# Performance work log

Hardware: AMD Instinct MI355X
Metric: run time of the kernel (lower is better)

The kernel has to match this reference:

```python
import jax, jax.numpy as jnp
import numpy as np


def setup_inputs() -> dict:
    B, C, N = 8, 512, 2048
    ks = jax.random.split(jax.random.key(0), 5)
    return {
        "src_embedding": jax.random.normal(ks[0], (B, C, N), jnp.float32),
        "tgt_embedding": jax.random.normal(ks[1], (B, C, N), jnp.float32),
        "src": jax.random.normal(ks[2], (B, 3, N), jnp.float32),
        "tgt": jax.random.normal(ks[3], (B, 3, N), jnp.float32),
        "temperature": jnp.ones((B, 1), jnp.float32),
        "gumbel_u": jax.random.uniform(ks[4], (B * N, N), jnp.float32),
    }


def reference(src_embedding, tgt_embedding, src, tgt, temperature, gumbel_u):
    B, C, N = src_embedding.shape
    # cross-attention scores: [B, N, N]
    scores = jnp.einsum('bcn,bcm->bnm', src_embedding, tgt_embedding) / jnp.sqrt(jnp.float32(C))
    scores = scores.reshape(B * N, N)
    tau = jnp.repeat(temperature.reshape(B, 1, 1), N, axis=1).reshape(-1, 1)  # [B*N, 1]
    # gumbel-softmax (hard=True, straight-through)
    u = jnp.clip(gumbel_u, 1e-6, 1.0 - 1e-6)
    g = -jnp.log(-jnp.log(u))
    y_soft = jax.nn.softmax((scores + g) / tau, axis=-1)
    idx = jnp.argmax(y_soft, axis=-1)
    y_hard = jax.nn.one_hot(idx, N, dtype=y_soft.dtype)
    scores_st = y_hard - jax.lax.stop_gradient(y_soft) + y_soft
    scores_st = scores_st.reshape(B, N, N)
    # soft correspondences: tgt @ scores^T -> [B, 3, N]
    src_corr = jnp.einsum('bcm,bnm->bcn', tgt, scores_st)
    src_mean = src.mean(axis=2, keepdims=True)
    corr_mean = src_corr.mean(axis=2, keepdims=True)
    src_c = src - src_mean
    corr_c = src_corr - corr_mean
    # 3x3 covariance per batch
    H = jnp.einsum('bcn,bdn->bcd', src_c, corr_c)
    uS, s, vh = jnp.linalg.svd(H)
    v = jnp.swapaxes(vh, -1, -2)
    uT = jnp.swapaxes(uS, -1, -2)
    r = v @ uT
    det = jax.lax.stop_gradient(jnp.linalg.det(r))  # torch code uses .item(): constant
    d = jnp.stack([jnp.ones_like(det), jnp.ones_like(det), det], axis=-1)  # [B, 3]
    R = (v * d[:, None, :]) @ uT  # v @ diag([1,1,det]) @ u^T
    t = jnp.einsum('bij,bjk->bik', -R, src_mean) + corr_mean
    return R, t.reshape(B, 3)
```

## Files before the change

kernel.cpp:

```cpp
#include <hip/hip_runtime.h>
#include <hip/hip_fp16.h>
#include <math.h>

#define NB 8
#define NC 512
#define NN 2048

typedef __attribute__((ext_vector_type(8))) _Float16 f16x8;
typedef __attribute__((ext_vector_type(4))) float f32x4;

union U8 { uint32_t u[4]; f16x8 v; };

__device__ __forceinline__ unsigned f2mono(float v) {
    unsigned b = __float_as_uint(v);
    return (b & 0x80000000u) ? ~b : (b | 0x80000000u);
}

__device__ __forceinline__ uint32_t packsplit(float a) {
    __half h = __float2half(a);
    float hf = __half2float(h);
    __half lo = __float2half(a - hf);
    return (uint32_t)__half_as_ushort(h) | ((uint32_t)__half_as_ushort(lo) << 16);
}

extern "C" __global__ __launch_bounds__(256, 2)
void scores_argmax(const float* __restrict__ srcE,
                   const float* __restrict__ tgtE,
                   const float* __restrict__ gum,
                   const float* __restrict__ temp,
                   unsigned long long* __restrict__ best)
{
    __shared__ uint32_t As[128 * 32];
    __shared__ uint32_t Bs[128 * 32];

    const int id = blockIdx.x;
    const int flat = (id & 7) * 256 + (id >> 3);
    const int mt = flat & 15;
    const int nt = (flat >> 4) & 15;
    const int b  = flat >> 8;
    const int n0 = nt * 128, m0 = mt * 128;

    const int tid = threadIdx.x;
    const int wv = tid >> 6;
    const int l  = tid & 63;
    const int wn = wv >> 1, wm = wv & 1;
    const int row16 = l & 15, h = l >> 4;

    const int snb = 4 * (tid & 31);
    const int skb = tid >> 5;
    const uint32_t sswz = (uint32_t)(tid & 7) << 2;

    const float* Ag = srcE + (size_t)b * NC * NN + n0 + snb;
    const float* Bg = tgtE + (size_t)b * NC * NN + m0 + snb;

    float4 pA[4], pB[4];
#pragma unroll
    for (int r = 0; r < 4; ++r) {
        pA[r] = *(const float4*)(Ag + (size_t)(skb + 8 * r) * NN);
        pB[r] = *(const float4*)(Bg + (size_t)(skb + 8 * r) * NN);
    }

    f32x4 acc[4][4];
#pragma unroll
    for (int i = 0; i < 4; ++i)
#pragma unroll
        for (int j = 0; j < 4; ++j)
            acc[i][j] = (f32x4){0.f, 0.f, 0.f, 0.f};

    for (int k0 = 0; k0 < NC; k0 += 32) {
        __syncthreads();
#pragma unroll
        for (int r = 0; r < 4; ++r) {
            const int k = skb + 8 * r;
            const uint32_t kx = (uint32_t)k ^ sswz;
            uint32_t* ap = &As[snb * 32 + kx];
            uint32_t* bq = &Bs[snb * 32 + kx];
            ap[0]  = packsplit(pA[r].x); ap[32] = packsplit(pA[r].y);
            ap[64] = packsplit(pA[r].z); ap[96] = packsplit(pA[r].w);
            bq[0]  = packsplit(pB[r].x); bq[32] = packsplit(pB[r].y);
            bq[64] = packsplit(pB[r].z); bq[96] = packsplit(pB[r].w);
        }
        if (k0 + 32 < NC) {
#pragma unroll
            for (int r = 0; r < 4; ++r) {
                pA[r] = *(const float4*)(Ag + (size_t)(k0 + 32 + skb + 8 * r) * NN);
                pB[r] = *(const float4*)(Bg + (size_t)(k0 + 32 + skb + 8 * r) * NN);
            }
        }
        __syncthreads();

        U8 bfh[4], bfl[4];
#pragma unroll
        for (int ms = 0; ms < 4; ++ms) {
            const int m_loc = wm * 64 + ms * 16 + row16;
            const uint32_t swz = (uint32_t)((ms * 4 + (row16 >> 2)) & 7) << 2;
            const int base = m_loc * 32;
            const uint4 r0 = *(const uint4*)&Bs[base + (((uint32_t)(h * 8 + 0)) ^ swz)];
            const uint4 r1 = *(const uint4*)&Bs[base + (((uint32_t)(h * 8 + 4)) ^ swz)];
            bfh[ms].u[0] = __builtin_amdgcn_perm(r0.y, r0.x, 0x05040100u);
            bfh[ms].u[1] = __builtin_amdgcn_perm(r0.w, r0.z, 0x05040100u);
            bfh[ms].u[2] = __builtin_amdgcn_perm(r1.y, r1.x, 0x05040100u);
            bfh[ms].u[3] = __builtin_amdgcn_perm(r1.w, r1.z, 0x05040100u);
            bfl[ms].u[0] = __builtin_amdgcn_perm(r0.y, r0.x, 0x07060302u);
            bfl[ms].u[1] = __builtin_amdgcn_perm(r0.w, r0.z, 0x07060302u);
            bfl[ms].u[2] = __builtin_amdgcn_perm(r1.y, r1.x, 0x07060302u);
            bfl[ms].u[3] = __builtin_amdgcn_perm(r1.w, r1.z, 0x07060302u);
        }

#pragma unroll
        for (int ns = 0; ns < 4; ++ns) {
            const int n_loc = wn * 64 + ns * 16 + row16;
            const uint32_t swz = (uint32_t)((ns * 4 + (row16 >> 2)) & 7) << 2;
            const int base = n_loc * 32;
            const uint4 r0 = *(const uint4*)&As[base + (((uint32_t)(h * 8 + 0)) ^ swz)];
            const uint4 r1 = *(const uint4*)&As[base + (((uint32_t)(h * 8 + 4)) ^ swz)];
            U8 ah, al;
            ah.u[0] = __builtin_amdgcn_perm(r0.y, r0.x, 0x05040100u);
            ah.u[1] = __builtin_amdgcn_perm(r0.w, r0.z, 0x05040100u);
            ah.u[2] = __builtin_amdgcn_perm(r1.y, r1.x, 0x05040100u);
            ah.u[3] = __builtin_amdgcn_perm(r1.w, r1.z, 0x05040100u);
            al.u[0] = __builtin_amdgcn_perm(r0.y, r0.x, 0x07060302u);
            al.u[1] = __builtin_amdgcn_perm(r0.w, r0.z, 0x07060302u);
            al.u[2] = __builtin_amdgcn_perm(r1.y, r1.x, 0x07060302u);
            al.u[3] = __builtin_amdgcn_perm(r1.w, r1.z, 0x07060302u);
#pragma unroll
            for (int ms = 0; ms < 4; ++ms) {
                acc[ns][ms] = __builtin_amdgcn_mfma_f32_16x16x32_f16(ah.v, bfh[ms].v, acc[ns][ms], 0, 0, 0);
                acc[ns][ms] = __builtin_amdgcn_mfma_f32_16x16x32_f16(al.v, bfh[ms].v, acc[ns][ms], 0, 0, 0);
                acc[ns][ms] = __builtin_amdgcn_mfma_f32_16x16x32_f16(ah.v, bfl[ms].v, acc[ns][ms], 0, 0, 0);
            }
        }
    }

    const float SCL = 0.044194173824159216f;
    const float tau = temp[b];
#pragma unroll
    for (int ns = 0; ns < 4; ++ns) {
#pragma unroll
        for (int reg = 0; reg < 4; ++reg) {
            const int n = n0 + wn * 64 + ns * 16 + h * 4 + reg;
            const float* gr = gum + ((size_t)(b * NN + n)) * NN + m0 + wm * 64 + row16;
            unsigned long long bp = 0ULL;
#pragma unroll
            for (int ms = 0; ms < 4; ++ms) {
                float u = gr[ms * 16];
                u = fminf(fmaxf(u, 1e-6f), 1.0f - 1e-6f);
                const float g = -logf(-logf(u));
                const float val = (acc[ns][ms][reg] * SCL + g) / tau;
                const int m = m0 + wm * 64 + ms * 16 + row16;
                const unsigned long long p =
                    ((unsigned long long)f2mono(val) << 32) | (unsigned)(NN - 1 - m);
                if (p > bp) bp = p;
            }
#pragma unroll
            for (int off = 8; off > 0; off >>= 1) {
                const unsigned long long o = __shfl_xor(bp, off, 16);
                if (o > bp) bp = o;
            }
            if (row16 == 0) atomicMax(&best[(size_t)b * NN + n], bp);
        }
    }
}

__device__ __forceinline__ double det3(const double M[3][3]) {
    return M[0][0] * (M[1][1] * M[2][2] - M[1][2] * M[2][1])
         - M[0][1] * (M[1][0] * M[2][2] - M[1][2] * M[2][0])
         + M[0][2] * (M[1][0] * M[2][1] - M[1][1] * M[2][0]);
}

extern "C" __global__ __launch_bounds__(256)
void assemble(const float* __restrict__ src, const float* __restrict__ tgt,
              const unsigned long long* __restrict__ best, float* __restrict__ out)
{
    const int b = blockIdx.x;
    const int tid = threadIdx.x;
    float P[9] = {}, Ss[3] = {}, Sc[3] = {};
    for (int n = tid; n < NN; n += 256) {
        const int m = (NN - 1) - (int)(unsigned)(best[(size_t)b * NN + n] & 0xffffffffu);
        float sv[3], cv[3];
#pragma unroll
        for (int c = 0; c < 3; ++c) {
            sv[c] = src[((size_t)b * 3 + c) * NN + n];
            cv[c] = tgt[((size_t)b * 3 + c) * NN + m];
            Ss[c] += sv[c];
            Sc[c] += cv[c];
        }
#pragma unroll
        for (int c = 0; c < 3; ++c)
#pragma unroll
            for (int d = 0; d < 3; ++d)
                P[c * 3 + d] = fmaf(sv[c], cv[d], P[c * 3 + d]);
    }

    float vals[15];
#pragma unroll
    for (int i = 0; i < 9; ++i) vals[i] = P[i];
#pragma unroll
    for (int i = 0; i < 3; ++i) { vals[9 + i] = Ss[i]; vals[12 + i] = Sc[i]; }

    __shared__ float red[4][15];
    const int lane = tid & 63, wv = tid >> 6;
#pragma unroll
    for (int i = 0; i < 15; ++i) {
        float v = vals[i];
        for (int off = 32; off > 0; off >>= 1) v += __shfl_down(v, off, 64);
        if (lane == 0) red[wv][i] = v;
    }
    __syncthreads();

    if (tid == 0) {
        double tot[15];
        for (int i = 0; i < 15; ++i)
            tot[i] = (double)red[0][i] + red[1][i] + red[2][i] + red[3][i];
        double smean[3], cmean[3], H[3][3];
        for (int c = 0; c < 3; ++c) { smean[c] = tot[9 + c] / NN; cmean[c] = tot[12 + c] / NN; }
        for (int c = 0; c < 3; ++c)
            for (int d = 0; d < 3; ++d)
                H[c][d] = tot[c * 3 + d] - tot[9 + c] * tot[12 + d] / NN;

        double W[3][3], V[3][3];
        for (int i = 0; i < 3; ++i)
            for (int j = 0; j < 3; ++j) { W[i][j] = H[i][j]; V[i][j] = (i == j) ? 1.0 : 0.0; }
        for (int sweep = 0; sweep < 60; ++sweep) {
            double offsum = 0.0;
            for (int p = 0; p < 2; ++p)
                for (int q = p + 1; q < 3; ++q) {
                    double al = 0, be = 0, ga = 0;
                    for (int r = 0; r < 3; ++r) {
                        al += W[r][p] * W[r][p];
                        be += W[r][q] * W[r][q];
                        ga += W[r][p] * W[r][q];
                    }
                    offsum += fabs(ga);
                    if (fabs(ga) <= 1e-15 * sqrt(al * be)) continue;
                    double zeta = (be - al) / (2.0 * ga);
                    double t = copysign(1.0, zeta) / (fabs(zeta) + sqrt(1.0 + zeta * zeta));
                    double c = 1.0 / sqrt(1.0 + t * t), s = c * t;
                    for (int r = 0; r < 3; ++r) {
                        double wp = W[r][p], wq = W[r][q];
                        W[r][p] = c * wp - s * wq;
                        W[r][q] = s * wp + c * wq;
                        double vp = V[r][p], vq = V[r][q];
                        V[r][p] = c * vp - s * vq;
                        V[r][q] = s * vp + c * vq;
                    }
                }
            if (offsum < 1e-13) break;
        }
        double S[3];
        for (int i = 0; i < 3; ++i)
            S[i] = sqrt(W[0][i] * W[0][i] + W[1][i] * W[1][i] + W[2][i] * W[2][i]);
        for (int i = 0; i < 2; ++i) {
            int mx = i;
            for (int j = i + 1; j < 3; ++j) if (S[j] > S[mx]) mx = j;
            if (mx != i) {
                double tS = S[i]; S[i] = S[mx]; S[mx] = tS;
                for (int r = 0; r < 3; ++r) {
                    double tw = W[r][i]; W[r][i] = W[r][mx]; W[r][mx] = tw;
                    double tv = V[r][i]; V[r][i] = V[r][mx]; V[r][mx] = tv;
                }
            }
        }
        double U[3][3];
        for (int i = 0; i < 3; ++i) {
            if (S[i] > 1e-12 * S[0] && S[i] > 0.0) {
                for (int r = 0; r < 3; ++r) U[r][i] = W[r][i] / S[i];
            } else {
                double ux = U[1][0] * U[2][1] - U[2][0] * U[1][1];
                double uy = U[2][0] * U[0][1] - U[0][0] * U[2][1];
                double uz = U[0][0] * U[1][1] - U[1][0] * U[0][1];
                double nr = sqrt(ux * ux + uy * uy + uz * uz);
                if (nr < 1e-30) { ux = 1.0; uy = 0.0; uz = 0.0; nr = 1.0; }
                U[0][i] = ux / nr; U[1][i] = uy / nr; U[2][i] = uz / nr;
            }
        }
        double r_[3][3];
        for (int i = 0; i < 3; ++i)
            for (int j = 0; j < 3; ++j)
                r_[i][j] = V[i][0] * U[j][0] + V[i][1] * U[j][1] + V[i][2] * U[j][2];
        double det = det3(r_);
        double R[3][3];
        for (int i = 0; i < 3; ++i)
            for (int j = 0; j < 3; ++j)
                R[i][j] = V[i][0] * U[j][0] + V[i][1] * U[j][1] + det * V[i][2] * U[j][2];
        double t_[3];
        for (int i = 0; i < 3; ++i)
            t_[i] = -(R[i][0] * smean[0] + R[i][1] * smean[1] + R[i][2] * smean[2]) + cmean[i];

        for (int i = 0; i < 3; ++i)
            for (int j = 0; j < 3; ++j)
                out[b * 9 + i * 3 + j] = (float)R[i][j];
        for (int i = 0; i < 3; ++i) out[NB * 9 + b * 3 + i] = (float)t_[i];
    }
}

extern "C" void kernel_launch(void* const* d_in, const int* in_sizes, int n_in,
                              void* d_out, int out_size, void* d_ws, size_t ws_size,
                              hipStream_t stream)
{
    const float* srcE = (const float*)d_in[0];
    const float* tgtE = (const float*)d_in[1];
    const float* src  = (const float*)d_in[2];
    const float* tgt  = (const float*)d_in[3];
    const float* temp = (const float*)d_in[4];
    const float* gum  = (const float*)d_in[5];
    float* out = (float*)d_out;
    unsigned long long* best = (unsigned long long*)d_ws;

    hipMemsetAsync(best, 0, (size_t)NB * NN * sizeof(unsigned long long), stream);

    scores_argmax<<<2048, 256, 0, stream>>>(srcE, tgtE, gum, temp, best);
    assemble<<<NB, 256, 0, stream>>>(src, tgt, best, out);
}
```

Baseline: 210.7 us.

## Prepack embeddings into swizzled fp16 hi/lo planes and stream via direct LDS loads

Adds a prepack kernel that splits the fp32 embeddings once into fp16 hi/lo planes, transposed to N-major rows with an XOR swizzle. A new GEMM+argmax kernel then streams those planes into double-buffered LDS with global_load_lds, one wave per plane, and runs three fp16 MFMAs per tile. This removes the per-tile fp32-to-fp16 split and register-staged LDS stores from the main loop and overlaps loads with compute. In exchange it adds an extra kernel pass that writes and rereads a large workspace, and it only runs when the workspace is big enough.

```diff
diff --git a/kernel.cpp b/kernel.cpp
--- a/kernel.cpp
+++ b/kernel.cpp
@@ -21,6 +21,177 @@
     float hf = __half2float(h);
     __half lo = __float2half(a - hf);
     return (uint32_t)__half_as_ushort(h) | ((uint32_t)__half_as_ushort(lo) << 16);
+}
+
+__device__ __forceinline__ void g2lds16(const void* g, void* l) {
+    __builtin_amdgcn_global_load_lds(
+        (const __attribute__((address_space(1))) void*)g,
+        (__attribute__((address_space(3))) void*)l, 16, 0, 0);
+}
+
+extern "C" __global__ __launch_bounds__(256)
+void prepack(const float* __restrict__ srcE, const float* __restrict__ tgtE,
+             unsigned short* __restrict__ hiA, unsigned short* __restrict__ loA,
+             unsigned short* __restrict__ hiB, unsigned short* __restrict__ loB)
+{
+    const float* in = blockIdx.y ? tgtE : srcE;
+    unsigned short* hi = blockIdx.y ? hiB : hiA;
+    unsigned short* lo = blockIdx.y ? loB : loA;
+    const int t  = blockIdx.x;
+    const int b  = t >> 7;
+    const int kt = (t >> 3) & 15;
+    const int nt = t & 7;
+    const int k0 = kt * 32, n0 = nt * 256;
+
+    const int n_l = threadIdx.x;
+    const int n   = n0 + n_l;
+    const int s2  = (n >> 1) & 3;
+    const float* gin = in + (size_t)b * (NC * NN) + (size_t)k0 * NN + n;
+
+    float v[32];
+#pragma unroll
+    for (int k = 0; k < 32; ++k) v[k] = gin[(size_t)k * NN];
+
+    uint32_t hw[16], lw[16];
+#pragma unroll
+    for (int j = 0; j < 16; ++j) {
+        __half h0 = __float2half(v[2*j]);
+        __half h1 = __float2half(v[2*j+1]);
+        float  d0 = v[2*j]   - __half2float(h0);
+        float  d1 = v[2*j+1] - __half2float(h1);
+        hw[j] = (uint32_t)__half_as_ushort(h0) | ((uint32_t)__half_as_ushort(h1) << 16);
+        lw[j] = (uint32_t)__half_as_ushort(__float2half(d0)) |
+                ((uint32_t)__half_as_ushort(__float2half(d1)) << 16);
+    }
+    const size_t rowbase = ((size_t)b * NN + n) * NC;
+#pragma unroll
+    for (int o = 0; o < 4; ++o) {
+        const int P = kt * 4 + (o ^ s2);
+        uint4 qh, ql;
+        qh.x = hw[4*o+0]; qh.y = hw[4*o+1]; qh.z = hw[4*o+2]; qh.w = hw[4*o+3];
+        ql.x = lw[4*o+0]; ql.y = lw[4*o+1]; ql.z = lw[4*o+2]; ql.w = lw[4*o+3];
+        *(uint4*)(hi + rowbase + (size_t)P * 8) = qh;
+        *(uint4*)(lo + rowbase + (size_t)P * 8) = ql;
+    }
+}
+
+extern "C" __global__ __launch_bounds__(256, 2)
+void scores_argmax_fast(const unsigned short* __restrict__ hiA, const unsigned short* __restrict__ loA,
+                        const unsigned short* __restrict__ hiB, const unsigned short* __restrict__ loB,
+                        const float* __restrict__ gum, const float* __restrict__ temp,
+                        unsigned long long* __restrict__ best)
+{
+    __shared__ unsigned short lds[2][4][4096];
+
+    const int id = blockIdx.x;
+    const int flat = (id & 7) * 256 + (id >> 3);
+    const int mt = flat & 15;
+    const int nt = (flat >> 4) & 15;
+    const int b  = flat >> 8;
+    const int n0 = nt * 128, m0 = mt * 128;
+
+    const int tid = threadIdx.x;
+    const int wv = tid >> 6;
+    const int l  = tid & 63;
+    const int wn = wv >> 1, wm = wv & 1;
+    const int row16 = l & 15, h = l >> 4;
+    const int s2 = (row16 >> 1) & 3;
+    const int fo = ((h ^ s2) * 8);
+
+    const unsigned short* gp;
+    int pan;
+    if (wv == 0)      { gp = hiA; pan = n0; }
+    else if (wv == 1) { gp = loA; pan = n0; }
+    else if (wv == 2) { gp = hiB; pan = m0; }
+    else              { gp = loB; pan = m0; }
+    gp += ((size_t)b * NN + pan) * NC;
+    const unsigned short* gl = gp + (size_t)(l >> 2) * NC + (l & 3) * 8;
+
+#define STAGE(T, BUF) do {                                                   \
+    const unsigned short* s_ = gl + (size_t)(T) * 32;                        \
+    _Pragma("unroll")                                                        \
+    for (int c_ = 0; c_ < 8; ++c_)                                           \
+        g2lds16(s_ + (size_t)c_ * 16 * NC, &lds[BUF][wv][c_ * 512]);         \
+} while (0)
+
+    f32x4 acc[4][4];
+#pragma unroll
+    for (int i = 0; i < 4; ++i)
+#pragma unroll
+        for (int j = 0; j < 4; ++j)
+            acc[i][j] = (f32x4){0.f, 0.f, 0.f, 0.f};
+
+#define COMPUTE(BUF) do {                                                    \
+    const unsigned short* L_ = &lds[BUF][0][0];                              \
+    f16x8 bh_[4], bl_[4];                                                    \
+    _Pragma("unroll")                                                        \
+    for (int ms = 0; ms < 4; ++ms) {                                         \
+        const int r_ = wm * 64 + ms * 16 + row16;                            \
+        bh_[ms] = *(const f16x8*)&L_[2 * 4096 + r_ * 32 + fo];               \
+        bl_[ms] = *(const f16x8*)&L_[3 * 4096 + r_ * 32 + fo];               \
+    }                                                                        \
+    _Pragma("unroll")                                                        \
+    for (int ns = 0; ns < 4; ++ns) {                                         \
+        const int r_ = wn * 64 + ns * 16 + row16;                            \
+        const f16x8 ah_ = *(const f16x8*)&L_[0 * 4096 + r_ * 32 + fo];       \
+        const f16x8 al_ = *(const f16x8*)&L_[1 * 4096 + r_ * 32 + fo];       \
+        _Pragma("unroll")                                                    \
+        for (int ms = 0; ms < 4; ++ms) {                                     \
+            acc[ns][ms] = __builtin_amdgcn_mfma_f32_16x16x32_f16(ah_, bh_[ms], acc[ns][ms], 0, 0, 0); \
+            acc[ns][ms] = __builtin_amdgcn_mfma_f32_16x16x32_f16(al_, bh_[ms], acc[ns][ms], 0, 0, 0); \
+            acc[ns][ms] = __builtin_amdgcn_mfma_f32_16x16x32_f16(ah_, bl_[ms], acc[ns][ms], 0, 0, 0); \
+        }                                                                    \
+    }                                                                        \
+} while (0)
+
+    STAGE(0, 0);
+    for (int t = 0; t < 15; ++t) {
+        STAGE(t + 1, (t + 1) & 1);
+        asm volatile("s_waitcnt vmcnt(8)" ::: "memory");
+        __builtin_amdgcn_sched_barrier(0);
+        __builtin_amdgcn_s_barrier();
+        asm volatile("" ::: "memory");
+        COMPUTE(t & 1);
+        asm volatile("" ::: "memory");
+        __builtin_amdgcn_s_barrier();
+        asm volatile("" ::: "memory");
+    }
+    asm volatile("s_waitcnt vmcnt(0)" ::: "memory");
+    __builtin_amdgcn_sched_barrier(0);
+    __builtin_amdgcn_s_barrier();
+    asm volatile("" ::: "memory");
+    COMPUTE(1);
+
+    const float SCL = 0.044194173824159216f;
+    const float tau = temp[b];
+#pragma unroll
+    for (int ns = 0; ns < 4; ++ns) {
+#pragma unroll
+        for (int reg = 0; reg < 4; ++reg) {
+            const int n = n0 + wn * 64 + ns * 16 + h * 4 + reg;
+            const float* gr = gum + ((size_t)(b * NN + n)) * NN + m0 + wm * 64 + row16;
+            unsigned long long bp = 0ULL;
+#pragma unroll
+            for (int ms = 0; ms < 4; ++ms) {
+                float u = gr[ms * 16];
+                u = fminf(fmaxf(u, 1e-6f), 1.0f - 1e-6f);
+                const float g = -logf(-logf(u));
+                const float val = (acc[ns][ms][reg] * SCL + g) / tau;
+                const int m = m0 + wm * 64 + ms * 16 + row16;
+                const unsigned long long p =
+                    ((unsigned long long)f2mono(val) << 32) | (unsigned)(NN - 1 - m);
+                if (p > bp) bp = p;
+            }
+#pragma unroll
+            for (int off = 8; off > 0; off >>= 1) {
+                const unsigned long long o = __shfl_xor(bp, off, 16);
+                if (o > bp) bp = o;
+            }
+            if (row16 == 0) atomicMax(&best[(size_t)b * NN + n], bp);
+        }
+    }
+#undef STAGE
+#undef COMPUTE
 }
 
 extern "C" __global__ __launch_bounds__(256, 2)
@@ -32,7 +203,6 @@
 {
     __shared__ uint32_t As[128 * 32];
     __shared__ uint32_t Bs[128 * 32];
-
     const int id = blockIdx.x;
     const int flat = (id & 7) * 256 + (id >> 3);
     const int mt = flat & 15;
@@ -307,8 +477,19 @@
     float* out = (float*)d_out;
     unsigned long long* best = (unsigned long long*)d_ws;
 
-    hipMemsetAsync(best, 0, (size_t)NB * NN * sizeof(unsigned long long), stream);
-
-    scores_argmax<<<2048, 256, 0, stream>>>(srcE, tgtE, gum, temp, best);
+    (void)hipMemsetAsync(best, 0, (size_t)NB * NN * sizeof(unsigned long long), stream);
+
+    const size_t PLANE = (size_t)NB * NN * NC;
+    const size_t NEED  = 131072 + 4 * PLANE * sizeof(unsigned short);
+    if (ws_size >= NEED) {
+        unsigned short* hiA = (unsigned short*)((char*)d_ws + 131072);
+        unsigned short* loA = hiA + PLANE;
+        unsigned short* hiB = loA + PLANE;
+        unsigned short* loB = hiB + PLANE;
+        prepack<<<dim3(1024, 2), 256, 0, stream>>>(srcE, tgtE, hiA, loA, hiB, loB);
+        scores_argmax_fast<<<2048, 256, 0, stream>>>(hiA, loA, hiB, loB, gum, temp, best);
+    } else {
+        scores_argmax<<<2048, 256, 0, stream>>>(srcE, tgtE, gum, temp, best);
+    }
     assemble<<<NB, 256, 0, stream>>>(src, tgt, best, out);
 }
```

Result: slower. 234.2 us (+11.2%).
